# Performance work log

Hardware: AMD Instinct MI355X
Metric: run time of the kernel (lower is better)

Reference implementation:

```python
import jax, jax.numpy as jnp
import numpy as np

M, H, F, T, IT, NUM_SEM = 256, 256, 256, 4, 2, 50
NEG = jnp.float32(-1e30)


def _lin(k, fi, fo):
    kw, kb = jax.random.split(k)
    s = 1.0 / np.sqrt(fi)
    W = jax.random.uniform(kw, (fi, fo), minval=-s, maxval=s, dtype=jnp.float32)
    b = jax.random.uniform(kb, (fo,), minval=-s, maxval=s, dtype=jnp.float32)
    return W, b


def setup_inputs() -> dict:
    key = jax.random.key(0)
    ks = jax.random.split(key, 16)
    parent_feature = jax.random.normal(ks[0], (1, F), dtype=jnp.float32)
    gt_children_code = jax.random.normal(ks[1], (1, 16), dtype=jnp.float32)
    gt_num_code = jax.random.normal(ks[2], (1, 10), dtype=jnp.float32)
    W_parent, b_parent = _lin(ks[3], F + 26, H * M)
    W_exists, b_exists = _lin(ks[4], H, 1)
    W_sem, b_sem = _lin(ks[5], H, NUM_SEM)
    W_el, b_el = _lin(ks[6], 2 * H, H)          # mlp_edge_latent
    s = 1.0 / np.sqrt(H)
    W_ee = jax.random.uniform(ks[7], (T, H), minval=-s, maxval=s, dtype=jnp.float32)  # stacked mlp_edge_exists
    b_ee = jax.random.uniform(ks[8], (T,), minval=-s, maxval=s, dtype=jnp.float32)
    s2 = 1.0 / np.sqrt(3 * H + T)
    W_ne = jax.random.uniform(ks[9], (IT, 3 * H + T, H), minval=-s2, maxval=s2, dtype=jnp.float32)  # node_edge_op
    b_ne = jax.random.uniform(ks[10], (IT, H), minval=-s2, maxval=s2, dtype=jnp.float32)
    W_child, b_child = _lin(ks[11], H * (IT + 1), H)
    W_child2, b_child2 = _lin(ks[12], H, F)
    return dict(parent_feature=parent_feature, gt_children_code=gt_children_code,
                gt_num_code=gt_num_code, W_parent=W_parent, b_parent=b_parent,
                W_exists=W_exists, b_exists=b_exists, W_sem=W_sem, b_sem=b_sem,
                W_el=W_el, b_el=b_el, W_ee=W_ee, b_ee=b_ee, W_ne=W_ne, b_ne=b_ne,
                W_child=W_child, b_child=b_child, W_child2=W_child2, b_child2=b_child2)


def reference(parent_feature, gt_children_code, gt_num_code, W_parent, b_parent,
              W_exists, b_exists, W_sem, b_sem, W_el, b_el, W_ee, b_ee,
              W_ne, b_ne, W_child, b_child, W_child2, b_child2):
    x = jnp.concatenate([parent_feature, gt_children_code, gt_num_code], axis=1)  # [1, F+26]
    child = jax.nn.relu(x @ W_parent + b_parent).reshape(1, M, H)
    exists_logits = child @ W_exists + b_exists                   # [1, M, 1]
    cf = child[0]                                                 # [M, H]
    # edge latents: relu(Linear(cat(cf_i, cf_j))) without materializing [M,M,2H]
    a = cf @ W_el[:H]
    b2 = cf @ W_el[H:]
    el = jax.nn.relu(a[:, None, :] + b2[None, :, :] + b_el)       # [M, M, H]
    ee = jnp.einsum('mnh,th->mnt', el, W_ee) + b_ee               # [M, M, T]
    # fixed edge set: candidate edges where type-logit>0 and both endpoints exist
    node_ok = exists_logits[0, :, 0] > 0                          # [M]
    mask = (ee > 0) & node_ok[:, None, None] & node_ok[None, :, None]  # [M, M, T]
    has_edges = mask.any()
    iter_feats = [cf]
    for i in range(IT):
        W = W_ne[i]
        Ws, Wd, We, Wt = W[:H], W[H:2 * H], W[2 * H:3 * H], W[3 * H:]
        pre = (cf @ Ws)[:, None, :] + (cf @ Wd)[None, :, :] \
              + jnp.einsum('mnh,hk->mnk', el, We) + b_ne[i]       # [M, M, H]
        # one-hot edge-type logit contribution: etl[e,t]=ee[i,j,t] only at the edge's type
        feats = jax.nn.relu(pre[:, :, None, :] + jnp.einsum('mnt,th->mnth', ee, Wt))  # [M,M,T,H]
        # scatter_max over source node i with zero-initialized output
        new = jnp.max(jnp.where(mask[..., None], feats, NEG), axis=(1, 2))  # [M, H]
        new = jnp.maximum(new, 0.0)
        cf = jnp.where(has_edges, new, cf)
        iter_feats.append(cf)
    cfc = jnp.concatenate(iter_feats, axis=1)                     # [M, H*(IT+1)]
    ch = jax.nn.relu(cfc @ W_child + b_child)                     # [M, H]
    child_sem_logits = (ch @ W_sem + b_sem)[None]                 # [1, M, NUM_SEM]
    child_feats = jax.nn.relu(ch @ W_child2 + b_child2)[None]     # [1, M, F]
    return child_feats, child_sem_logits, exists_logits, ee[None]
```

## Files before the change

kernel.cpp:

```cpp
#include <hip/hip_runtime.h>
#include <hip/hip_bf16.h>
#include <stdint.h>

#define NEGV -1e30f

typedef __attribute__((ext_vector_type(8))) __bf16 bf16x8;
typedef __attribute__((ext_vector_type(4))) float f32x4;

__device__ __forceinline__ uint16_t f2bfu(float f){
  __hip_bfloat16 h = __float2bfloat16(f);
  return *reinterpret_cast<const uint16_t*>(&h);
}

__device__ __forceinline__ void dev_transpose(
  const float* __restrict__ in, __hip_bfloat16* __restrict__ out,
  int K, int N, int ktiles, int b, int tid, float* t)
{
  int kt = b % ktiles, nt = b / ktiles;
  int k0 = kt*64, n0 = nt*64;
  int c = tid & 63, rg = tid >> 6;
  #pragma unroll
  for (int rr = 0; rr < 16; ++rr){
    int row = rg + rr*4;
    t[row*65 + c] = in[(k0+row)*N + n0 + c];
  }
  __syncthreads();
  #pragma unroll
  for (int rr = 0; rr < 16; ++rr){
    int row = rg + rr*4;
    out[(n0+row)*K + k0 + c] = __float2bfloat16(t[c*65 + row]);
  }
}

__global__ __launch_bounds__(256) void k_front(
    const float* __restrict__ pf, const float* __restrict__ gc,
    const float* __restrict__ gn, const float* __restrict__ Wp,
    const float* __restrict__ Wne, const float* __restrict__ Wch,
    const float* __restrict__ Wc2, const float* __restrict__ Wsem,
    float* __restrict__ pchild, __hip_bfloat16* __restrict__ WeT,
    __hip_bfloat16* __restrict__ WchT, __hip_bfloat16* __restrict__ Wc2T,
    __hip_bfloat16* __restrict__ WsemT)
{
  __shared__ float sh[64*65];
  int bid = blockIdx.x, tid = threadIdx.x;
  if (bid < 512){
    int jb = bid & 63, ks = bid >> 6;
    int i0 = ks*36, i1 = (i0+36 < 282) ? i0+36 : 282;
    if (tid < i1-i0){
      int i = i0 + tid;
      sh[tid] = (i < 256) ? pf[i] : ((i < 272) ? gc[i-256] : gn[i-272]);
    }
    __syncthreads();
    int j0 = jb*1024 + tid*4;
    f32x4 acc = {0,0,0,0};
    #pragma unroll 6
    for (int i = i0; i < i1; ++i){
      f32x4 w = *reinterpret_cast<const f32x4*>(Wp + i*65536 + j0);
      float x = sh[i-i0];
      acc[0] = fmaf(x, w[0], acc[0]);
      acc[1] = fmaf(x, w[1], acc[1]);
      acc[2] = fmaf(x, w[2], acc[2]);
      acc[3] = fmaf(x, w[3], acc[3]);
    }
    *reinterpret_cast<f32x4*>(pchild + ks*65536 + j0) = acc;
  } else if (bid < 544){
    int b = bid - 512; int it = b >> 4;
    dev_transpose(Wne + it*197632 + 512*256, WeT + it*65536, 256, 256, 4, b & 15, tid, sh);
  } else if (bid < 592){
    dev_transpose(Wch, WchT, 768, 256, 12, bid - 544, tid, sh);
  } else if (bid < 608){
    dev_transpose(Wc2, Wc2T, 256, 256, 4, bid - 592, tid, sh);
  } else {
    int b = bid - 608;
    int j = b*4 + (tid>>6), c = tid & 63;
    float v = (c < 50) ? Wsem[j*50+c] : 0.f;
    WsemT[c*256 + j] = __float2bfloat16(v);
  }
}

__global__ __launch_bounds__(256) void k_reduce_ab(
  const float* __restrict__ pchild, const float* __restrict__ bp,
  const float* __restrict__ Wex, const float* __restrict__ bex,
  const float* __restrict__ Wel,
  float* __restrict__ cf, __hip_bfloat16* __restrict__ cfcb,
  float* __restrict__ exout, int* __restrict__ ok, int* __restrict__ flag,
  float* __restrict__ a, float* __restrict__ b2)
{
  __shared__ float shmem[2][256];
  int bid = blockIdx.x, tid = threadIdx.x;
  if (bid < 256){
    int m = bid;
    int j = m*256 + tid;
    float s = bp[j];
    #pragma unroll
    for (int ks = 0; ks < 8; ++ks) s += pchild[ks*65536 + j];
    s = fmaxf(s, 0.f);
    cf[j] = s;
    cfcb[m*768 + tid] = __float2bfloat16(s);
    shmem[0][tid] = s * Wex[tid];
    __syncthreads();
    float* red = shmem[0];
    for (int st = 128; st > 0; st >>= 1){ if (tid < st) red[tid] += red[tid+st]; __syncthreads(); }
    if (tid == 0){
      float logit = red[0] + bex[0];
      exout[m] = logit;
      ok[m] = logit > 0.f ? 1 : 0;
      if (m == 0) *flag = 0;
    }
  } else {
    int b = bid - 256;
    int sel = b >> 7; int m0 = (b & 127)*2;
    #pragma unroll
    for (int r = 0; r < 2; ++r){
      int j = (m0+r)*256 + tid;
      float s = bp[j];
      #pragma unroll
      for (int ks = 0; ks < 8; ++ks) s += pchild[ks*65536 + j];
      shmem[r][tid] = fmaxf(s, 0.f);
    }
    __syncthreads();
    const float* W = Wel + sel*65536;
    float acc0 = 0.f, acc1 = 0.f;
    #pragma unroll 8
    for (int j = 0; j < 256; ++j){
      float w = W[j*256+tid];
      acc0 = fmaf(shmem[0][j], w, acc0);
      acc1 = fmaf(shmem[1][j], w, acc1);
    }
    float* dst = sel ? b2 : a;
    dst[m0*256+tid] = acc0;
    dst[(m0+1)*256+tid] = acc1;
  }
}

__global__ __launch_bounds__(256) void k_b2t(
  const float* __restrict__ b2, float* __restrict__ b2T)
{
  __shared__ float t[64][65];
  int bt = blockIdx.x;
  int n0 = (bt & 3)*64, h0 = (bt >> 2)*64;
  int tid = threadIdx.x; int c = tid & 63, rg = tid >> 6;
  #pragma unroll
  for (int rr = 0; rr < 16; ++rr){
    int row = rg + rr*4;
    t[row][c] = b2[(size_t)(n0+row)*256 + h0 + c];
  }
  __syncthreads();
  #pragma unroll
  for (int rr = 0; rr < 16; ++rr){
    int row = rg + rr*4;
    b2T[(size_t)(h0+row)*256 + n0 + c] = t[c][row];
  }
}

__global__ __launch_bounds__(256) void k_ee_part(
  const float* __restrict__ a, const float* __restrict__ b2T,
  const float* __restrict__ bel, const float* __restrict__ Wee,
  float* __restrict__ pee)
{
  __shared__ float wee[4][128];
  __shared__ float ac[128];
  int bid = blockIdx.x; int m = bid & 255; int hs = bid >> 8;
  int tid = threadIdx.x;
  int h0 = hs*128;
  if (tid < 128){
    ac[tid] = a[m*256 + h0 + tid] + bel[h0 + tid];
    wee[0][tid] = Wee[      h0 + tid];
    wee[1][tid] = Wee[256 + h0 + tid];
  } else {
    int t = tid - 128;
    wee[2][t] = Wee[512 + h0 + t];
    wee[3][t] = Wee[768 + h0 + t];
  }
  __syncthreads();
  int n = tid;
  float e0 = 0.f, e1 = 0.f, e2 = 0.f, e3 = 0.f;
  #pragma unroll 8
  for (int h = 0; h < 128; ++h){
    float el = fmaxf(ac[h] + b2T[(h0+h)*256 + n], 0.f);
    e0 = fmaf(el, wee[0][h], e0);
    e1 = fmaf(el, wee[1][h], e1);
    e2 = fmaf(el, wee[2][h], e2);
    e3 = fmaf(el, wee[3][h], e3);
  }
  f32x4 p; p[0]=e0; p[1]=e1; p[2]=e2; p[3]=e3;
  *reinterpret_cast<f32x4*>(pee + ((hs*256+m)*256 + n)*4) = p;
}

__global__ __launch_bounds__(256) void k_eecomb_sd0(
  const float* __restrict__ pee, const float* __restrict__ bee,
  const int* __restrict__ ok, float* __restrict__ eemask,
  float* __restrict__ eeout, int* __restrict__ flag,
  const float* __restrict__ cf, const float* __restrict__ Wne,
  const float* __restrict__ bne, float* __restrict__ sp, float* __restrict__ d)
{
  __shared__ float cfs[2][256];
  int bid = blockIdx.x, tid = threadIdx.x;
  if (bid < 256){
    int m = bid, n = tid;
    f32x4 p0 = *reinterpret_cast<const f32x4*>(pee + ((0*256+m)*256 + n)*4);
    f32x4 p1 = *reinterpret_cast<const f32x4*>(pee + ((1*256+m)*256 + n)*4);
    float e0 = bee[0] + p0[0] + p1[0];
    float e1 = bee[1] + p0[1] + p1[1];
    float e2 = bee[2] + p0[2] + p1[2];
    float e3 = bee[3] + p0[3] + p1[3];
    int idx = (m*256+n)*4;
    f32x4 eo; eo[0]=e0; eo[1]=e1; eo[2]=e2; eo[3]=e3;
    *reinterpret_cast<f32x4*>(eeout + idx) = eo;
    int okmn = ok[m] & ok[n];
    f32x4 em;
    em[0] = (okmn && e0 > 0.f) ? e0 : NEGV;
    em[1] = (okmn && e1 > 0.f) ? e1 : NEGV;
    em[2] = (okmn && e2 > 0.f) ? e2 : NEGV;
    em[3] = (okmn && e3 > 0.f) ? e3 : NEGV;
    *reinterpret_cast<f32x4*>(eemask + idx) = em;
    if (em[0] > -1e29f || em[1] > -1e29f || em[2] > -1e29f || em[3] > -1e29f) atomicOr(flag, 1);
  } else {
    int b = bid - 256;
    int sel = b >> 7; int m0 = (b & 127)*2;
    cfs[0][tid] = cf[m0*256 + tid];
    cfs[1][tid] = cf[(m0+1)*256 + tid];
    __syncthreads();
    const float* W = Wne + sel*65536;
    float bias = sel ? 0.f : bne[tid];
    float acc0 = bias, acc1 = bias;
    #pragma unroll 8
    for (int j = 0; j < 256; ++j){
      float w = W[j*256+tid];
      acc0 = fmaf(cfs[0][j], w, acc0);
      acc1 = fmaf(cfs[1][j], w, acc1);
    }
    float* dst = sel ? d : sp;
    dst[m0*256+tid] = acc0;
    dst[(m0+1)*256+tid] = acc1;
  }
}

__global__ __launch_bounds__(256) void k_sd(
  const float* __restrict__ cf, const float* __restrict__ Wne,
  const float* __restrict__ bne, float* __restrict__ sp, float* __restrict__ d, int it)
{
  __shared__ float cfs[2][256];
  int bid = blockIdx.x; int sel = bid >> 7; int m0 = (bid & 127)*2; int tid = threadIdx.x;
  cfs[0][tid] = cf[m0*256 + tid];
  cfs[1][tid] = cf[(m0+1)*256 + tid];
  __syncthreads();
  const float* W = Wne + it*197632 + sel*65536;
  float bias = sel ? 0.f : bne[it*256+tid];
  float acc0 = bias, acc1 = bias;
  #pragma unroll 8
  for (int j = 0; j < 256; ++j){
    float w = W[j*256+tid];
    acc0 = fmaf(cfs[0][j], w, acc0);
    acc1 = fmaf(cfs[1][j], w, acc1);
  }
  float* dst = sel ? d : sp;
  dst[m0*256+tid] = acc0;
  dst[(m0+1)*256+tid] = acc1;
}

__global__ __launch_bounds__(256,2) void k_fused_v3(
  const float* __restrict__ a, const float* __restrict__ bel,
  const float* __restrict__ b2, const __hip_bfloat16* __restrict__ wet,
  const float* __restrict__ sp, const float* __restrict__ dmat,
  const float* __restrict__ eemask, const float* __restrict__ Wne_it,
  float* __restrict__ cf, __hip_bfloat16* __restrict__ cfcb,
  const int* __restrict__ flag, int it)
{
  __shared__ __attribute__((aligned(16))) char weS[32768];
  __shared__ __attribute__((aligned(16))) char elS[32768];
  __shared__ float acs[256];
  __shared__ float red[4][64];
  int bid = blockIdx.x; int m = bid >> 2, kc = bid & 3;
  int tid = threadIdx.x;
  acs[tid] = a[m*256+tid] + bel[tid];
  const char* wsrc = reinterpret_cast<const char*>(wet + kc*16384);
  #pragma unroll
  for (int p = 0; p < 8; ++p){
    int i = p*256 + tid;
    int row = i >> 5, colb = (i & 31) << 4;
    int byte = (row << 9) | colb;
    *reinterpret_cast<bf16x8*>(weS + (byte ^ ((row & 7) << 4))) =
      *reinterpret_cast<const bf16x8*>(wsrc + byte);
  }
  __syncthreads();

  int w = tid >> 6, l = tid & 63, l15 = l & 15, lg = l >> 4;
  float spv[4], wtv[4][4];
  #pragma unroll
  for (int kt = 0; kt < 4; ++kt){
    int kcol = kc*64 + kt*16 + l15;
    spv[kt] = sp[m*256+kcol];
    #pragma unroll
    for (int t = 0; t < 4; ++t) wtv[t][kt] = Wne_it[(768+t)*256 + kcol];
  }
  int rowb[4], rowx[4];
  #pragma unroll
  for (int kt = 0; kt < 4; ++kt){
    int row = kt*16 + l15;
    rowb[kt] = row << 9;
    rowx[kt] = (row & 7) << 4;
  }
  int arow = w*16 + l15;
  float runmax[4] = {NEGV, NEGV, NEGV, NEGV};

  for (int c = 0; c < 4; ++c){
    #pragma unroll
    for (int p = 0; p < 16; ++p){
      int idx = p*256 + tid;
      int row = idx >> 6;
      int h4 = (idx & 63) << 2;
      f32x4 bv = *reinterpret_cast<const f32x4*>(b2 + (size_t)(c*64+row)*256 + h4);
      f32x4 av = *reinterpret_cast<const f32x4*>(acs + h4);
      union { uint16_t u[4]; uint64_t d; } pk;
      #pragma unroll
      for (int j = 0; j < 4; ++j) pk.u[j] = f2bfu(fmaxf(av[j]+bv[j], 0.f));
      int byte = (row << 9) | (h4 << 1);
      *reinterpret_cast<uint64_t*>(elS + (byte ^ ((row & 7) << 4))) = pk.d;
    }
    __syncthreads();

    int nb = c*64 + w*16;
    f32x4 me[4];
    float dv[4][4];
    #pragma unroll
    for (int r = 0; r < 4; ++r){
      int n = nb + lg*4 + r;
      me[r] = *reinterpret_cast<const f32x4*>(eemask + (m*256+n)*4);
      const float* dr = dmat + n*256 + kc*64;
      #pragma unroll
      for (int kt = 0; kt < 4; ++kt) dv[r][kt] = dr[kt*16 + l15];
    }
    bf16x8 Af[8];
    #pragma unroll
    for (int kk = 0; kk < 8; ++kk)
      Af[kk] = *reinterpret_cast<const bf16x8*>(elS + (((arow << 9) | (kk*64 + lg*16)) ^ ((arow & 7) << 4)));

    f32x4 acc0 = {0,0,0,0}, acc1 = {0,0,0,0}, acc2 = {0,0,0,0}, acc3 = {0,0,0,0};
    #pragma unroll
    for (int kk = 0; kk < 8; ++kk){
      int cc = kk*64 + lg*16;
      bf16x8 B0 = *reinterpret_cast<const bf16x8*>(weS + ((rowb[0] + cc) ^ rowx[0]));
      bf16x8 B1 = *reinterpret_cast<const bf16x8*>(weS + ((rowb[1] + cc) ^ rowx[1]));
      bf16x8 B2 = *reinterpret_cast<const bf16x8*>(weS + ((rowb[2] + cc) ^ rowx[2]));
      bf16x8 B3 = *reinterpret_cast<const bf16x8*>(weS + ((rowb[3] + cc) ^ rowx[3]));
      acc0 = __builtin_amdgcn_mfma_f32_16x16x32_bf16(Af[kk], B0, acc0, 0, 0, 0);
      acc1 = __builtin_amdgcn_mfma_f32_16x16x32_bf16(Af[kk], B1, acc1, 0, 0, 0);
      acc2 = __builtin_amdgcn_mfma_f32_16x16x32_bf16(Af[kk], B2, acc2, 0, 0, 0);
      acc3 = __builtin_amdgcn_mfma_f32_16x16x32_bf16(Af[kk], B3, acc3, 0, 0, 0);
    }
    #pragma unroll
    for (int r = 0; r < 4; ++r){
      float Ed0 = acc0[r] + dv[r][0] + spv[0];
      float Ed1 = acc1[r] + dv[r][1] + spv[1];
      float Ed2 = acc2[r] + dv[r][2] + spv[2];
      float Ed3 = acc3[r] + dv[r][3] + spv[3];
      #pragma unroll
      for (int t = 0; t < 4; ++t){
        if (me[r][t] > -1e29f){
          runmax[0] = fmaxf(runmax[0], fmaf(me[r][t], wtv[t][0], Ed0));
          runmax[1] = fmaxf(runmax[1], fmaf(me[r][t], wtv[t][1], Ed1));
          runmax[2] = fmaxf(runmax[2], fmaf(me[r][t], wtv[t][2], Ed2));
          runmax[3] = fmaxf(runmax[3], fmaf(me[r][t], wtv[t][3], Ed3));
        }
      }
    }
    __syncthreads();
  }
  #pragma unroll
  for (int kt = 0; kt < 4; ++kt){
    float v = runmax[kt];
    v = fmaxf(v, __shfl_xor(v, 16));
    v = fmaxf(v, __shfl_xor(v, 32));
    if (l < 16) red[w][kt*16 + l] = v;
  }
  __syncthreads();
  if (tid < 64){
    float v = fmaxf(fmaxf(red[0][tid], red[1][tid]), fmaxf(red[2][tid], red[3][tid]));
    float nv = fmaxf(v, 0.f);
    int kcol = kc*64 + tid;
    float outv = (*flag) ? nv : cf[m*256+kcol];
    cf[m*256+kcol] = outv;
    cfcb[m*768 + 256*(it+1) + kcol] = __float2bfloat16(outv);
  }
}

__global__ __launch_bounds__(256) void k_final_mfma(
  const __hip_bfloat16* __restrict__ cfcb, const __hip_bfloat16* __restrict__ WchT,
  const float* __restrict__ bch, const __hip_bfloat16* __restrict__ Wc2T,
  const float* __restrict__ bc2, const __hip_bfloat16* __restrict__ WsemT,
  const float* __restrict__ bsem, float* __restrict__ feats_out,
  float* __restrict__ sem_out)
{
  __shared__ char chs[8192];
  int tid = threadIdx.x; int w = tid>>6, l = tid&63, l15 = l&15, lg = l>>4;
  int m0 = blockIdx.x*16;

  f32x4 acc[4] = {{0,0,0,0},{0,0,0,0},{0,0,0,0},{0,0,0,0}};
  const __hip_bfloat16* Aptr = cfcb + (m0 + l15)*768;
  #pragma unroll 2
  for (int ks = 0; ks < 24; ++ks){
    int k0 = ks*32 + lg*8;
    bf16x8 Af = *reinterpret_cast<const bf16x8*>(Aptr + k0);
    #pragma unroll
    for (int nt = 0; nt < 4; ++nt){
      int col = w*64 + nt*16 + l15;
      bf16x8 Bf = *reinterpret_cast<const bf16x8*>(WchT + col*768 + k0);
      acc[nt] = __builtin_amdgcn_mfma_f32_16x16x32_bf16(Af, Bf, acc[nt], 0, 0, 0);
    }
  }
  #pragma unroll
  for (int nt = 0; nt < 4; ++nt){
    int col = w*64 + nt*16 + l15;
    float bias = bch[col];
    #pragma unroll
    for (int r = 0; r < 4; ++r){
      int row = lg*4 + r;
      float v = fmaxf(acc[nt][r] + bias, 0.f);
      int byte = ((row*256 + col)*2) ^ ((row&7)<<4);
      *reinterpret_cast<__hip_bfloat16*>(chs + byte) = __float2bfloat16(v);
    }
  }
  __syncthreads();

  f32x4 accf[4] = {{0,0,0,0},{0,0,0,0},{0,0,0,0},{0,0,0,0}};
  f32x4 accs = {0,0,0,0};
  int cols_sem = w*16 + l15;
  #pragma unroll 2
  for (int ks = 0; ks < 8; ++ks){
    int k0 = ks*32 + lg*8;
    int byteA = (l15*512 + k0*2) ^ ((l15&7)<<4);
    bf16x8 Af = *reinterpret_cast<const bf16x8*>(chs + byteA);
    #pragma unroll
    for (int nt = 0; nt < 4; ++nt){
      int col = w*64 + nt*16 + l15;
      bf16x8 Bf = *reinterpret_cast<const bf16x8*>(Wc2T + col*256 + k0);
      accf[nt] = __builtin_amdgcn_mfma_f32_16x16x32_bf16(Af, Bf, accf[nt], 0, 0, 0);
    }
    bf16x8 Bs = *reinterpret_cast<const bf16x8*>(WsemT + cols_sem*256 + k0);
    accs = __builtin_amdgcn_mfma_f32_16x16x32_bf16(Af, Bs, accs, 0, 0, 0);
  }
  #pragma unroll
  for (int nt = 0; nt < 4; ++nt){
    int col = w*64 + nt*16 + l15;
    float bias = bc2[col];
    #pragma unroll
    for (int r = 0; r < 4; ++r){
      int row = m0 + lg*4 + r;
      feats_out[row*256 + col] = fmaxf(accf[nt][r] + bias, 0.f);
    }
  }
  if (cols_sem < 50){
    float bias = bsem[cols_sem];
    #pragma unroll
    for (int r = 0; r < 4; ++r){
      int row = m0 + lg*4 + r;
      sem_out[row*50 + cols_sem] = accs[r] + bias;
    }
  }
}

extern "C" void kernel_launch(void* const* d_in, const int* in_sizes, int n_in,
                              void* d_out, int out_size, void* d_ws, size_t ws_size,
                              hipStream_t stream)
{
  const float* pf  = (const float*)d_in[0];
  const float* gc  = (const float*)d_in[1];
  const float* gn  = (const float*)d_in[2];
  const float* Wp  = (const float*)d_in[3];
  const float* bp  = (const float*)d_in[4];
  const float* Wex = (const float*)d_in[5];
  const float* bex = (const float*)d_in[6];
  const float* Wsem= (const float*)d_in[7];
  const float* bsem= (const float*)d_in[8];
  const float* Wel = (const float*)d_in[9];
  const float* bel = (const float*)d_in[10];
  const float* Wee = (const float*)d_in[11];
  const float* bee = (const float*)d_in[12];
  const float* Wne = (const float*)d_in[13];
  const float* bne = (const float*)d_in[14];
  const float* Wch = (const float*)d_in[15];
  const float* bch = (const float*)d_in[16];
  const float* Wc2 = (const float*)d_in[17];
  const float* bc2 = (const float*)d_in[18];

  float* out = (float*)d_out;
  float* feats_out = out;
  float* sem_out   = out + 65536;
  float* ex_out    = out + 78336;
  float* ee_out    = out + 78592;

  char* ws = (char*)d_ws;
  float* cf    = (float*)(ws);
  float* a_    = (float*)(ws + ( 256u<<10));
  float* b2_   = (float*)(ws + ( 512u<<10));
  float* b2T   = (float*)(ws + ( 768u<<10));
  float* sp_   = (float*)(ws + (1024u<<10));
  float* dmat  = (float*)(ws + (1280u<<10));
  float* eem   = (float*)(ws + (1536u<<10));
  __hip_bfloat16* WeT   = (__hip_bfloat16*)(ws + (2560u<<10));
  __hip_bfloat16* cfcb  = (__hip_bfloat16*)(ws + (2816u<<10));
  __hip_bfloat16* WchT  = (__hip_bfloat16*)(ws + (3200u<<10));
  __hip_bfloat16* Wc2T  = (__hip_bfloat16*)(ws + (3584u<<10));
  __hip_bfloat16* WsemT = (__hip_bfloat16*)(ws + (3712u<<10));
  int* ok   = (int*)(ws + (3744u<<10));
  int* flag = ok + 256;
  float* pchild = (float*)(ws + (3776u<<10));
  float* pee    = pchild;

  k_front<<<672,256,0,stream>>>(pf,gc,gn,Wp,Wne,Wch,Wc2,Wsem,
                                pchild,WeT,WchT,Wc2T,WsemT);
  k_reduce_ab<<<512,256,0,stream>>>(pchild,bp,Wex,bex,Wel,cf,cfcb,ex_out,ok,flag,a_,b2_);
  k_b2t<<<16,256,0,stream>>>(b2_,b2T);
  k_ee_part<<<512,256,0,stream>>>(a_,b2T,bel,Wee,pee);
  k_eecomb_sd0<<<512,256,0,stream>>>(pee,bee,ok,eem,ee_out,flag,cf,Wne,bne,sp_,dmat);
  k_fused_v3<<<1024,256,0,stream>>>(a_,bel,b2_,WeT,sp_,dmat,eem,Wne,cf,cfcb,flag,0);
  k_sd<<<256,256,0,stream>>>(cf,Wne,bne,sp_,dmat,1);
  k_fused_v3<<<1024,256,0,stream>>>(a_,bel,b2_,WeT + 65536,sp_,dmat,eem,
                                    Wne + 197632,cf,cfcb,flag,1);
  k_final_mfma<<<16,256,0,stream>>>(cfcb,WchT,bch,Wc2T,bc2,WsemT,bsem,feats_out,sem_out);
}
```

Baseline: 150.2 us.

## Fuse b2 transpose into reduce kernel and prefetch b2 tiles into registers

Removes the separate k_b2t transpose launch by having k_reduce_ab write the transposed b2 directly, using strided scattered stores. In the fused iteration kernel, the next chunk of b2 is now loaded into 16 f32x4 registers right after the barrier, so global latency overlaps the MFMA work of the current chunk. This adds 64 registers of pressure under a launch bound of 2 blocks per CU, which may cause spills. The transposed stores are uncoalesced.

```diff
diff --git a/kernel.cpp b/kernel.cpp
--- a/kernel.cpp
+++ b/kernel.cpp
@@ -84,7 +84,7 @@
   const float* __restrict__ Wel,
   float* __restrict__ cf, __hip_bfloat16* __restrict__ cfcb,
   float* __restrict__ exout, int* __restrict__ ok, int* __restrict__ flag,
-  float* __restrict__ a, float* __restrict__ b2)
+  float* __restrict__ a, float* __restrict__ b2, float* __restrict__ b2T)
 {
   __shared__ float shmem[2][256];
   int bid = blockIdx.x, tid = threadIdx.x;
@@ -130,26 +130,10 @@
     float* dst = sel ? b2 : a;
     dst[m0*256+tid] = acc0;
     dst[(m0+1)*256+tid] = acc1;
-  }
-}
-
-__global__ __launch_bounds__(256) void k_b2t(
-  const float* __restrict__ b2, float* __restrict__ b2T)
-{
-  __shared__ float t[64][65];
-  int bt = blockIdx.x;
-  int n0 = (bt & 3)*64, h0 = (bt >> 2)*64;
-  int tid = threadIdx.x; int c = tid & 63, rg = tid >> 6;
-  #pragma unroll
-  for (int rr = 0; rr < 16; ++rr){
-    int row = rg + rr*4;
-    t[row][c] = b2[(size_t)(n0+row)*256 + h0 + c];
-  }
-  __syncthreads();
-  #pragma unroll
-  for (int rr = 0; rr < 16; ++rr){
-    int row = rg + rr*4;
-    b2T[(size_t)(h0+row)*256 + n0 + c] = t[c][row];
+    if (sel){
+      b2T[tid*256 + m0]   = acc0;
+      b2T[tid*256 + m0+1] = acc1;
+    }
   }
 }
 
@@ -259,7 +243,7 @@
   dst[(m0+1)*256+tid] = acc1;
 }
 
-__global__ __launch_bounds__(256,2) void k_fused_v3(
+__global__ __launch_bounds__(256,2) void k_fused_v4(
   const float* __restrict__ a, const float* __restrict__ bel,
   const float* __restrict__ b2, const __hip_bfloat16* __restrict__ wet,
   const float* __restrict__ sp, const float* __restrict__ dmat,
@@ -304,21 +288,38 @@
   int arow = w*16 + l15;
   float runmax[4] = {NEGV, NEGV, NEGV, NEGV};
 
+  int srow = tid >> 2;
+  f32x4 bv[16];
+  #pragma unroll
+  for (int p = 0; p < 16; ++p){
+    int idx = p*256 + tid;
+    int row = idx >> 6, h4 = (idx & 63) << 2;
+    bv[p] = *reinterpret_cast<const f32x4*>(b2 + (size_t)(row)*256 + h4);
+  }
+
   for (int c = 0; c < 4; ++c){
     #pragma unroll
     for (int p = 0; p < 16; ++p){
       int idx = p*256 + tid;
       int row = idx >> 6;
       int h4 = (idx & 63) << 2;
-      f32x4 bv = *reinterpret_cast<const f32x4*>(b2 + (size_t)(c*64+row)*256 + h4);
       f32x4 av = *reinterpret_cast<const f32x4*>(acs + h4);
       union { uint16_t u[4]; uint64_t d; } pk;
       #pragma unroll
-      for (int j = 0; j < 4; ++j) pk.u[j] = f2bfu(fmaxf(av[j]+bv[j], 0.f));
+      for (int j = 0; j < 4; ++j) pk.u[j] = f2bfu(fmaxf(av[j]+bv[p][j], 0.f));
       int byte = (row << 9) | (h4 << 1);
       *reinterpret_cast<uint64_t*>(elS + (byte ^ ((row & 7) << 4))) = pk.d;
     }
     __syncthreads();
+
+    if (c < 3){
+      #pragma unroll
+      for (int p = 0; p < 16; ++p){
+        int idx = p*256 + tid;
+        int row = idx >> 6, h4 = (idx & 63) << 2;
+        bv[p] = *reinterpret_cast<const f32x4*>(b2 + (size_t)((c+1)*64+row)*256 + h4);
+      }
+    }
 
     int nb = c*64 + w*16;
     f32x4 me[4];
@@ -510,13 +511,12 @@
 
   k_front<<<672,256,0,stream>>>(pf,gc,gn,Wp,Wne,Wch,Wc2,Wsem,
                                 pchild,WeT,WchT,Wc2T,WsemT);
-  k_reduce_ab<<<512,256,0,stream>>>(pchild,bp,Wex,bex,Wel,cf,cfcb,ex_out,ok,flag,a_,b2_);
-  k_b2t<<<16,256,0,stream>>>(b2_,b2T);
+  k_reduce_ab<<<512,256,0,stream>>>(pchild,bp,Wex,bex,Wel,cf,cfcb,ex_out,ok,flag,a_,b2_,b2T);
   k_ee_part<<<512,256,0,stream>>>(a_,b2T,bel,Wee,pee);
   k_eecomb_sd0<<<512,256,0,stream>>>(pee,bee,ok,eem,ee_out,flag,cf,Wne,bne,sp_,dmat);
-  k_fused_v3<<<1024,256,0,stream>>>(a_,bel,b2_,WeT,sp_,dmat,eem,Wne,cf,cfcb,flag,0);
+  k_fused_v4<<<1024,256,0,stream>>>(a_,bel,b2_,WeT,sp_,dmat,eem,Wne,cf,cfcb,flag,0);
   k_sd<<<256,256,0,stream>>>(cf,Wne,bne,sp_,dmat,1);
-  k_fused_v3<<<1024,256,0,stream>>>(a_,bel,b2_,WeT + 65536,sp_,dmat,eem,
+  k_fused_v4<<<1024,256,0,stream>>>(a_,bel,b2_,WeT + 65536,sp_,dmat,eem,
                                     Wne + 197632,cf,cfcb,flag,1);
   k_final_mfma<<<16,256,0,stream>>>(cfcb,WchT,bch,Wc2T,bc2,WsemT,bsem,feats_out,sem_out);
 }
```

New measurement: 145.5 us. 3.2% less time.
